# Performance work log

Measured on AMD Instinct MI355X. Metric: run time of the kernel, lower is better.

The kernel has to match this reference:

```python
import jax, jax.numpy as jnp
import numpy as np
from jax import lax

B, L, H, KSIZE = 8, 16384, 128, 65
PAD = KSIZE // 2  # 32; odd kernel keeps output length == L


def setup_inputs() -> dict:
    key = jax.random.key(0)
    kq, kk, kv, kw = jax.random.split(key, 4)
    Q = jax.random.normal(kq, (B, L, H), dtype=jnp.float32)
    K = jax.random.normal(kk, (B, L, H), dtype=jnp.float32)
    V = jax.random.normal(kv, (B, L, H), dtype=jnp.float32)
    # Conv1d weight [out_ch, in_ch, kernel], kaiming-like scale
    W = jax.random.normal(kw, (H, H, KSIZE), dtype=jnp.float32) / np.sqrt(H * KSIZE)
    return {"Q": Q, "K": K, "V": V, "W": W}


def reference(Q, K, V, W):
    # [B, L, H] -> [B, H, L] (channels-first, matching torch transpose(1,2))
    Qt = jnp.swapaxes(Q, 1, 2)
    Kt = jnp.swapaxes(K, 1, 2)
    Vt = jnp.swapaxes(V, 1, 2)
    # Conv1d over sequence dim; lax conv is cross-correlation like torch
    conv_q = lax.conv_general_dilated(
        Qt, W,
        window_strides=(1,),
        padding=[(PAD, PAD)],
        dimension_numbers=("NCH", "OIH", "NCH"),
    )  # [B, H, L]
    scores = conv_q * Kt                      # elementwise gate
    A = jax.nn.softmax(scores, axis=-1)       # softmax over sequence dim
    Z = A * Vt                                # weighted V (elementwise)
    return jnp.swapaxes(Z, 1, 2)              # back to [B, L, H]
```

## Files before the change

kernel.cpp:

```cpp
#include <hip/hip_runtime.h>
#include <stdint.h>

#define BATCH 8
#define LSEQ 16384
#define HDIM 128
#define KSZ 65
#define PADW 32
#define LH (LSEQ*HDIM)
#define TL 256
#define NROWS (TL + 2*PADW)
#define LBLKS (LSEQ/TL)
#define EXP_SHIFT 20.0f

#define WS_WBF_OFF 4096

typedef __attribute__((ext_vector_type(8))) short bf16x8;
typedef __attribute__((ext_vector_type(4))) short bf16x4;
typedef __attribute__((ext_vector_type(16))) float f32x16;

__device__ __forceinline__ unsigned short f2bf(float f) {
  unsigned int u = __float_as_uint(f);
  return (unsigned short)((u + 0x7FFFu + ((u >> 16) & 1u)) >> 16);
}

__global__ __launch_bounds__(256) void wcvt_kernel(const float* __restrict__ W,
                                                   unsigned short* __restrict__ Wbf) {
  __shared__ float lw[KSZ*HDIM];
  const int o = blockIdx.x;
  const float* src = W + (size_t)o * (HDIM*KSZ);
  for (int t = threadIdx.x; t < HDIM*KSZ; t += 256) lw[t] = src[t];
  __syncthreads();
  const int ob  = o >> 5;
  const int l31 = o & 31;
  for (int idx = threadIdx.x; idx < KSZ*HDIM; idx += 256) {
    const int k = idx >> 7;
    const int i = idx & 127;
    const int kk  = i >> 4;
    const int hi2 = (i >> 3) & 1;
    const int e   = i & 7;
    const size_t dst = ((((size_t)(k*4 + ob)*8 + kk)*2 + hi2)*32 + l31)*8 + e;
    Wbf[dst] = f2bf(lw[i*KSZ + k]);
  }
}

__global__ __launch_bounds__(512, 4) void conv_gate_kernel(
    const float* __restrict__ Qm, const float* __restrict__ Km,
    const unsigned short* __restrict__ Wfrag,
    float* __restrict__ Eout, float* __restrict__ gsum) {

  __shared__ __align__(16) unsigned short Qs[NROWS*HDIM];

  const int tid  = threadIdx.x;
  const int lane = tid & 63;
  const int w    = tid >> 6;
  const int wr   = w >> 1;
  const int wc   = w & 1;
  const int l31  = lane & 31;
  const int hi2  = lane >> 5;

  const int bx = blockIdx.x;
  const int b  = bx >> 6;
  const int l0 = (bx & 63) << 8;

  {
    const int r0 = tid >> 5;
    const int c4 = (tid & 31) << 2;
    const float* qbase = Qm + (size_t)b*LH + c4;
#pragma unroll
    for (int it = 0; it < NROWS/16; ++it) {
      const int r = it*16 + r0;
      const int grow = l0 - PADW + r;
      bf16x4 pk = {0, 0, 0, 0};
      if (grow >= 0 && grow < LSEQ) {
        const float4 qv = *(const float4*)(qbase + (size_t)grow*HDIM);
        pk[0] = (short)f2bf(qv.x); pk[1] = (short)f2bf(qv.y);
        pk[2] = (short)f2bf(qv.z); pk[3] = (short)f2bf(qv.w);
      }
      *(bf16x4*)(&Qs[r*HDIM + (c4 ^ ((r & 15) << 3))]) = pk;
    }
  }

  const unsigned short* pb = Wfrag + (size_t)(wc*2)*4096 + hi2*256 + l31*8;

  f32x16 acc[2][2] = {};

  __syncthreads();

  const int arow0 = wr*64 + l31;
  for (int k = 0; k < KSZ; ++k) {
    const unsigned short* pk = pb + (size_t)k*16384;
    const int r0 = k + arow0;
    const int r1 = r0 + 32;
    const int xa0 = (r0 & 15) << 3, xa1 = (r1 & 15) << 3;
#pragma unroll
    for (int kk = 0; kk < 8; ++kk) {
      const int i0 = kk*16 + hi2*8;
      const bf16x8 a0 = *(const bf16x8*)(&Qs[r0*HDIM + (i0 ^ xa0)]);
      const bf16x8 a1 = *(const bf16x8*)(&Qs[r1*HDIM + (i0 ^ xa1)]);
      const bf16x8 b0 = *(const bf16x8*)(pk + kk*512);
      const bf16x8 b1 = *(const bf16x8*)(pk + 4096 + kk*512);
      __builtin_amdgcn_s_setprio(1);
      acc[0][0] = __builtin_amdgcn_mfma_f32_32x32x16_bf16(a0, b0, acc[0][0], 0, 0, 0);
      acc[0][1] = __builtin_amdgcn_mfma_f32_32x32x16_bf16(a0, b1, acc[0][1], 0, 0, 0);
      acc[1][0] = __builtin_amdgcn_mfma_f32_32x32x16_bf16(a1, b0, acc[1][0], 0, 0, 0);
      acc[1][1] = __builtin_amdgcn_mfma_f32_32x32x16_bf16(a1, b1, acc[1][1], 0, 0, 0);
      __builtin_amdgcn_s_setprio(0);
    }
  }

  float psum[2] = {0.f, 0.f};
#pragma unroll
  for (int mf = 0; mf < 2; ++mf) {
#pragma unroll
    for (int r = 0; r < 16; ++r) {
      const int row = wr*64 + mf*32 + (r & 3) + 8*(r >> 2) + 4*hi2;
      const size_t gb = (size_t)b*LH + (size_t)(l0 + row)*HDIM + wc*64 + l31;
#pragma unroll
      for (int nf = 0; nf < 2; ++nf) {
        const float s = acc[mf][nf][r] * Km[gb + nf*32];
        const float e = __expf(s - EXP_SHIFT);
        Eout[gb + nf*32] = e;
        psum[nf] += e;
      }
    }
  }
  psum[0] += __shfl_xor(psum[0], 32);
  psum[1] += __shfl_xor(psum[1], 32);
  if (hi2 == 0) {
    atomicAdd(&gsum[b*HDIM + wc*64 + l31],      psum[0]);
    atomicAdd(&gsum[b*HDIM + wc*64 + 32 + l31], psum[1]);
  }
}

__global__ __launch_bounds__(256) void finalize_kernel(float* __restrict__ out,
                                                       const float* __restrict__ V,
                                                       const float* __restrict__ gsum) {
  const int total4 = (BATCH*LH) >> 2;
  const int stride = gridDim.x * blockDim.x;
  for (int f = blockIdx.x*blockDim.x + threadIdx.x; f < total4; f += stride) {
    const float4 e = ((const float4*)out)[f];
    const float4 v = ((const float4*)V)[f];
    const int e0 = f << 2;
    const float* gs = gsum + ((e0 >> 21) << 7) + (e0 & 127);
    float4 z;
    z.x = e.x * v.x / gs[0];
    z.y = e.y * v.y / gs[1];
    z.z = e.z * v.z / gs[2];
    z.w = e.w * v.w / gs[3];
    ((float4*)out)[f] = z;
  }
}

extern "C" void kernel_launch(void* const* d_in, const int* in_sizes, int n_in,
                              void* d_out, int out_size, void* d_ws, size_t ws_size,
                              hipStream_t stream) {
  (void)in_sizes; (void)n_in; (void)out_size; (void)ws_size;
  const float* Q = (const float*)d_in[0];
  const float* K = (const float*)d_in[1];
  const float* V = (const float*)d_in[2];
  const float* W = (const float*)d_in[3];
  float* out  = (float*)d_out;
  float* gsum = (float*)d_ws;
  unsigned short* Wbf = (unsigned short*)((char*)d_ws + WS_WBF_OFF);

  hipMemsetAsync(d_ws, 0, BATCH*HDIM*sizeof(float), stream);
  wcvt_kernel<<<HDIM, 256, 0, stream>>>(W, Wbf);
  conv_gate_kernel<<<BATCH*LBLKS, 512, 0, stream>>>(Q, K, Wbf, out, gsum);
  finalize_kernel<<<2048, 256, 0, stream>>>(out, V, gsum);
}
```

Measured before the change: 335.4 us.

## Stage conv weights into LDS with async global_load_lds ring buffer

Weight fragments were previously read straight from global memory by every wave on each tap. They are now streamed into a 4-slot LDS ring with direct global-to-LDS loads issued two phases ahead, with vmcnt waits and barriers between phases. The weight layout is reordered into half-k phases to suit this, and A/B fragments are batched in registers before the MFMAs. The goal is to cut redundant global/L2 traffic and hide load latency, at the cost of more LDS per block (occupancy hint drops from 4 to 2), a barrier every phase, and reliance on vmcnt ordering for correctness.

```diff
diff --git a/kernel.cpp b/kernel.cpp
--- a/kernel.cpp
+++ b/kernel.cpp
@@ -11,6 +11,8 @@
 #define NROWS (TL + 2*PADW)
 #define LBLKS (LSEQ/TL)
 #define EXP_SHIFT 20.0f
+#define NPH (2*KSZ)
+#define HB 8192
 
 #define WS_WBF_OFF 4096
 
@@ -36,19 +38,36 @@
     const int k = idx >> 7;
     const int i = idx & 127;
     const int kk  = i >> 4;
+    const int kkh = kk >> 2;
+    const int kk2 = kk & 3;
     const int hi2 = (i >> 3) & 1;
     const int e   = i & 7;
-    const size_t dst = ((((size_t)(k*4 + ob)*8 + kk)*2 + hi2)*32 + l31)*8 + e;
+    const size_t dst = (size_t)(k*2 + kkh)*HB + ob*2048 + kk2*512 + hi2*256 + l31*8 + e;
     Wbf[dst] = f2bf(lw[i*KSZ + k]);
   }
 }
 
-__global__ __launch_bounds__(512, 4) void conv_gate_kernel(
+__device__ __forceinline__ void stage_half(const unsigned short* __restrict__ Wbf, int ph,
+                                           unsigned short* dst, int w, int lane) {
+  const char* gbase = (const char*)(Wbf + (size_t)ph * HB);
+  char* lbase = (char*)dst;
+#pragma unroll
+  for (int r = 0; r < 2; ++r) {
+    const int off = r*8192 + w*1024;
+    __builtin_amdgcn_global_load_lds(
+        (const __attribute__((address_space(1))) unsigned int*)(gbase + off + lane*16),
+        (__attribute__((address_space(3))) unsigned int*)(lbase + off),
+        16, 0, 0);
+  }
+}
+
+__global__ __launch_bounds__(512, 2) void conv_gate_kernel(
     const float* __restrict__ Qm, const float* __restrict__ Km,
     const unsigned short* __restrict__ Wfrag,
     float* __restrict__ Eout, float* __restrict__ gsum) {
 
   __shared__ __align__(16) unsigned short Qs[NROWS*HDIM];
+  __shared__ __align__(16) unsigned short Ws[4*HB];
 
   const int tid  = threadIdx.x;
   const int lane = tid & 63;
@@ -80,31 +99,48 @@
     }
   }
 
-  const unsigned short* pb = Wfrag + (size_t)(wc*2)*4096 + hi2*256 + l31*8;
+  stage_half(Wfrag, 0, &Ws[0*HB], w, lane);
+  stage_half(Wfrag, 1, &Ws[1*HB], w, lane);
 
   f32x16 acc[2][2] = {};
 
   __syncthreads();
 
   const int arow0 = wr*64 + l31;
+  const int bo0 = (wc*2+0)*2048 + hi2*256 + l31*8;
+  const int bo1 = (wc*2+1)*2048 + hi2*256 + l31*8;
+
   for (int k = 0; k < KSZ; ++k) {
-    const unsigned short* pk = pb + (size_t)k*16384;
     const int r0 = k + arow0;
     const int r1 = r0 + 32;
     const int xa0 = (r0 & 15) << 3, xa1 = (r1 & 15) << 3;
 #pragma unroll
-    for (int kk = 0; kk < 8; ++kk) {
-      const int i0 = kk*16 + hi2*8;
-      const bf16x8 a0 = *(const bf16x8*)(&Qs[r0*HDIM + (i0 ^ xa0)]);
-      const bf16x8 a1 = *(const bf16x8*)(&Qs[r1*HDIM + (i0 ^ xa1)]);
-      const bf16x8 b0 = *(const bf16x8*)(pk + kk*512);
-      const bf16x8 b1 = *(const bf16x8*)(pk + 4096 + kk*512);
+    for (int kkh = 0; kkh < 2; ++kkh) {
+      const int p = k*2 + kkh;
+      asm volatile("s_waitcnt vmcnt(2)" ::: "memory");
+      if (p + 2 < NPH)
+        stage_half(Wfrag, p + 2, &Ws[((p + 2) & 3) * HB], w, lane);
+      const unsigned short* hb = &Ws[(p & 3) * HB];
+
+      bf16x8 a0[4], a1[4], b0[4], b1[4];
+#pragma unroll
+      for (int kk2 = 0; kk2 < 4; ++kk2) {
+        const int i0 = (kkh*4 + kk2)*16 + hi2*8;
+        a0[kk2] = *(const bf16x8*)(&Qs[r0*HDIM + (i0 ^ xa0)]);
+        a1[kk2] = *(const bf16x8*)(&Qs[r1*HDIM + (i0 ^ xa1)]);
+        b0[kk2] = *(const bf16x8*)(hb + bo0 + kk2*512);
+        b1[kk2] = *(const bf16x8*)(hb + bo1 + kk2*512);
+      }
       __builtin_amdgcn_s_setprio(1);
-      acc[0][0] = __builtin_amdgcn_mfma_f32_32x32x16_bf16(a0, b0, acc[0][0], 0, 0, 0);
-      acc[0][1] = __builtin_amdgcn_mfma_f32_32x32x16_bf16(a0, b1, acc[0][1], 0, 0, 0);
-      acc[1][0] = __builtin_amdgcn_mfma_f32_32x32x16_bf16(a1, b0, acc[1][0], 0, 0, 0);
-      acc[1][1] = __builtin_amdgcn_mfma_f32_32x32x16_bf16(a1, b1, acc[1][1], 0, 0, 0);
+#pragma unroll
+      for (int kk2 = 0; kk2 < 4; ++kk2) {
+        acc[0][0] = __builtin_amdgcn_mfma_f32_32x32x16_bf16(a0[kk2], b0[kk2], acc[0][0], 0, 0, 0);
+        acc[0][1] = __builtin_amdgcn_mfma_f32_32x32x16_bf16(a0[kk2], b1[kk2], acc[0][1], 0, 0, 0);
+        acc[1][0] = __builtin_amdgcn_mfma_f32_32x32x16_bf16(a1[kk2], b0[kk2], acc[1][0], 0, 0, 0);
+        acc[1][1] = __builtin_amdgcn_mfma_f32_32x32x16_bf16(a1[kk2], b1[kk2], acc[1][1], 0, 0, 0);
+      }
       __builtin_amdgcn_s_setprio(0);
+      __builtin_amdgcn_s_barrier();
     }
   }
 
```

Result: faster. 323.9 us (-3.4%).

## Stage conv weight taps into LDS with double-buffered async loads and split-K warps

Applied to the files above, without the earlier changes.

Weight fragments for each tap are now copied into a double-buffered LDS slot with global_load_lds, overlapping the next tap's load with the current tap's MFMAs. Previously each wave read them straight from global memory. The warp layout changes so each wave computes a 128x64 output tile over half of the input channels. The two halves are reduced through LDS before the exp and gate epilogue. This raises LDS use to 144 KB and lowers occupancy to 2 blocks, and it adds a barrier per tap.

```diff
diff --git a/kernel.cpp b/kernel.cpp
--- a/kernel.cpp
+++ b/kernel.cpp
@@ -11,6 +11,7 @@
 #define NROWS (TL + 2*PADW)
 #define LBLKS (LSEQ/TL)
 #define EXP_SHIFT 20.0f
+#define SLOT 16384
 
 #define WS_WBF_OFF 4096
 
@@ -38,23 +39,39 @@
     const int kk  = i >> 4;
     const int hi2 = (i >> 3) & 1;
     const int e   = i & 7;
-    const size_t dst = ((((size_t)(k*4 + ob)*8 + kk)*2 + hi2)*32 + l31)*8 + e;
+    const size_t dst = (size_t)k*SLOT + kk*2048 + ob*512 + hi2*256 + l31*8 + e;
     Wbf[dst] = f2bf(lw[i*KSZ + k]);
   }
 }
 
-__global__ __launch_bounds__(512, 4) void conv_gate_kernel(
+__device__ __forceinline__ void stage_tap(const unsigned short* __restrict__ gsrc,
+                                          char* lbase, int w, int lane) {
+  const char* gb = (const char*)gsrc;
+#pragma unroll
+  for (int r = 0; r < 4; ++r) {
+    const int off = r*8192 + w*1024;
+    __builtin_amdgcn_global_load_lds(
+        (const __attribute__((address_space(1))) unsigned int*)(gb + off + lane*16),
+        (__attribute__((address_space(3))) unsigned int*)(lbase + off),
+        16, 0, 0);
+  }
+}
+
+__global__ __launch_bounds__(512, 2) void conv_gate_kernel(
     const float* __restrict__ Qm, const float* __restrict__ Km,
     const unsigned short* __restrict__ Wfrag,
     float* __restrict__ Eout, float* __restrict__ gsum) {
 
-  __shared__ __align__(16) unsigned short Qs[NROWS*HDIM];
+  __shared__ __align__(16) char smem[147456];
+  unsigned short* Qs = (unsigned short*)smem;
+  char* WsBase = smem + 81920;
 
   const int tid  = threadIdx.x;
   const int lane = tid & 63;
   const int w    = tid >> 6;
-  const int wr   = w >> 1;
-  const int wc   = w & 1;
+  const int ks   = w & 1;
+  const int wc   = (w >> 1) & 1;
+  const int wr   = w >> 2;
   const int l31  = lane & 31;
   const int hi2  = lane >> 5;
 
@@ -80,55 +97,103 @@
     }
   }
 
-  const unsigned short* pb = Wfrag + (size_t)(wc*2)*4096 + hi2*256 + l31*8;
-
-  f32x16 acc[2][2] = {};
+  stage_tap(Wfrag, WsBase, w, lane);
+
+  f32x16 acc[4][2] = {};
 
   __syncthreads();
 
-  const int arow0 = wr*64 + l31;
+  const int arow0 = wr*128 + l31;
+  const int bbase = (wc*2)*512 + lane*8;
+
+#define LOADC(c, A0,A1,A2,A3,B0,B1) { \
+    const int i0 = (ks*64 + (c)*16 + hi2*8) ^ xa; \
+    A0 = *(const bf16x8*)(&Qs[(rb     )*HDIM + i0]); \
+    A1 = *(const bf16x8*)(&Qs[(rb + 32)*HDIM + i0]); \
+    A2 = *(const bf16x8*)(&Qs[(rb + 64)*HDIM + i0]); \
+    A3 = *(const bf16x8*)(&Qs[(rb + 96)*HDIM + i0]); \
+    B0 = *(const bf16x8*)(&slot[(ks*4 + (c))*2048 + bbase]); \
+    B1 = *(const bf16x8*)(&slot[(ks*4 + (c))*2048 + bbase + 512]); \
+  }
+#define MM(A0,A1,A2,A3,B0,B1) \
+    acc[0][0] = __builtin_amdgcn_mfma_f32_32x32x16_bf16(A0, B0, acc[0][0], 0, 0, 0); \
+    acc[0][1] = __builtin_amdgcn_mfma_f32_32x32x16_bf16(A0, B1, acc[0][1], 0, 0, 0); \
+    acc[1][0] = __builtin_amdgcn_mfma_f32_32x32x16_bf16(A1, B0, acc[1][0], 0, 0, 0); \
+    acc[1][1] = __builtin_amdgcn_mfma_f32_32x32x16_bf16(A1, B1, acc[1][1], 0, 0, 0); \
+    acc[2][0] = __builtin_amdgcn_mfma_f32_32x32x16_bf16(A2, B0, acc[2][0], 0, 0, 0); \
+    acc[2][1] = __builtin_amdgcn_mfma_f32_32x32x16_bf16(A2, B1, acc[2][1], 0, 0, 0); \
+    acc[3][0] = __builtin_amdgcn_mfma_f32_32x32x16_bf16(A3, B0, acc[3][0], 0, 0, 0); \
+    acc[3][1] = __builtin_amdgcn_mfma_f32_32x32x16_bf16(A3, B1, acc[3][1], 0, 0, 0);
+
   for (int k = 0; k < KSZ; ++k) {
-    const unsigned short* pk = pb + (size_t)k*16384;
-    const int r0 = k + arow0;
-    const int r1 = r0 + 32;
-    const int xa0 = (r0 & 15) << 3, xa1 = (r1 & 15) << 3;
-#pragma unroll
-    for (int kk = 0; kk < 8; ++kk) {
-      const int i0 = kk*16 + hi2*8;
-      const bf16x8 a0 = *(const bf16x8*)(&Qs[r0*HDIM + (i0 ^ xa0)]);
-      const bf16x8 a1 = *(const bf16x8*)(&Qs[r1*HDIM + (i0 ^ xa1)]);
-      const bf16x8 b0 = *(const bf16x8*)(pk + kk*512);
-      const bf16x8 b1 = *(const bf16x8*)(pk + 4096 + kk*512);
-      __builtin_amdgcn_s_setprio(1);
-      acc[0][0] = __builtin_amdgcn_mfma_f32_32x32x16_bf16(a0, b0, acc[0][0], 0, 0, 0);
-      acc[0][1] = __builtin_amdgcn_mfma_f32_32x32x16_bf16(a0, b1, acc[0][1], 0, 0, 0);
-      acc[1][0] = __builtin_amdgcn_mfma_f32_32x32x16_bf16(a1, b0, acc[1][0], 0, 0, 0);
-      acc[1][1] = __builtin_amdgcn_mfma_f32_32x32x16_bf16(a1, b1, acc[1][1], 0, 0, 0);
-      __builtin_amdgcn_s_setprio(0);
-    }
-  }
-
-  float psum[2] = {0.f, 0.f};
-#pragma unroll
-  for (int mf = 0; mf < 2; ++mf) {
-#pragma unroll
-    for (int r = 0; r < 16; ++r) {
-      const int row = wr*64 + mf*32 + (r & 3) + 8*(r >> 2) + 4*hi2;
-      const size_t gb = (size_t)b*LH + (size_t)(l0 + row)*HDIM + wc*64 + l31;
-#pragma unroll
-      for (int nf = 0; nf < 2; ++nf) {
-        const float s = acc[mf][nf][r] * Km[gb + nf*32];
-        const float e = __expf(s - EXP_SHIFT);
-        Eout[gb + nf*32] = e;
-        psum[nf] += e;
+    const unsigned short* slot = (const unsigned short*)(WsBase + (k & 1)*32768);
+    if (k < KSZ-1)
+      stage_tap(Wfrag + (size_t)(k+1)*SLOT, WsBase + ((k+1) & 1)*32768, w, lane);
+
+    const int rb = k + arow0;
+    const int xa = (rb & 15) << 3;
+
+    bf16x8 a0,a1,a2,a3,b0,b1, c0,c1,c2,c3,d0,d1;
+    LOADC(0, a0,a1,a2,a3,b0,b1)
+    LOADC(1, c0,c1,c2,c3,d0,d1)
+    MM(a0,a1,a2,a3,b0,b1)
+    LOADC(2, a0,a1,a2,a3,b0,b1)
+    MM(c0,c1,c2,c3,d0,d1)
+    LOADC(3, c0,c1,c2,c3,d0,d1)
+    MM(a0,a1,a2,a3,b0,b1)
+    MM(c0,c1,c2,c3,d0,d1)
+
+    asm volatile("s_waitcnt vmcnt(0)" ::: "memory");
+    __builtin_amdgcn_s_barrier();
+  }
+#undef LOADC
+#undef MM
+
+  float* red = (float*)smem;
+  const int widx = wr*2 + wc;
+  float* reg = red + widx*8192 + lane*4;
+  if (ks == 1) {
+#pragma unroll
+    for (int e4 = 0; e4 < 32; ++e4) {
+      const int mfr = e4 >> 3, nf = (e4 >> 2) & 1, r4 = (e4 & 3) << 2;
+      float4 v;
+      v.x = acc[mfr][nf][r4];   v.y = acc[mfr][nf][r4+1];
+      v.z = acc[mfr][nf][r4+2]; v.w = acc[mfr][nf][r4+3];
+      *(float4*)(reg + e4*256) = v;
+    }
+  }
+  __syncthreads();
+
+  if (ks == 0) {
+#pragma unroll
+    for (int e4 = 0; e4 < 32; ++e4) {
+      const int mfr = e4 >> 3, nf = (e4 >> 2) & 1, r4 = (e4 & 3) << 2;
+      const float4 v = *(const float4*)(reg + e4*256);
+      acc[mfr][nf][r4]   += v.x; acc[mfr][nf][r4+1] += v.y;
+      acc[mfr][nf][r4+2] += v.z; acc[mfr][nf][r4+3] += v.w;
+    }
+    float psum[2] = {0.f, 0.f};
+#pragma unroll
+    for (int mfr = 0; mfr < 4; ++mfr) {
+#pragma unroll
+      for (int r = 0; r < 16; ++r) {
+        const int row = wr*128 + mfr*32 + (r & 3) + 8*(r >> 2) + 4*hi2;
+        const size_t gb = (size_t)b*LH + (size_t)(l0 + row)*HDIM + wc*64 + l31;
+#pragma unroll
+        for (int nf = 0; nf < 2; ++nf) {
+          const float s = acc[mfr][nf][r] * Km[gb + nf*32];
+          const float e = __expf(s - EXP_SHIFT);
+          Eout[gb + nf*32] = e;
+          psum[nf] += e;
+        }
       }
     }
-  }
-  psum[0] += __shfl_xor(psum[0], 32);
-  psum[1] += __shfl_xor(psum[1], 32);
-  if (hi2 == 0) {
-    atomicAdd(&gsum[b*HDIM + wc*64 + l31],      psum[0]);
-    atomicAdd(&gsum[b*HDIM + wc*64 + 32 + l31], psum[1]);
+    psum[0] += __shfl_xor(psum[0], 32);
+    psum[1] += __shfl_xor(psum[1], 32);
+    if (hi2 == 0) {
+      atomicAdd(&gsum[b*HDIM + wc*64 + l31],      psum[0]);
+      atomicAdd(&gsum[b*HDIM + wc*64 + 32 + l31], psum[1]);
+    }
   }
 }
 
```

After: 279.9 us (median of 2 runs). -16.5%, faster.

## Stage conv weights into LDS with double-buffered async loads and split-K waves

Applied to the files above, without the earlier changes.

Each wave used to read the bf16 weight fragments straight from global memory inside the 65-tap loop. Now the weights are repacked into half-tap slots and streamed into a double-buffered LDS area with global_load_lds, prefetching the next slot while MFMAs run on the current one. The sequence tile shrinks from 256 to 128 rows, and the 8 waves split the reduction dimension in two, with the partial accumulators combined through LDS before the exp/gate epilogue. This adds a barrier per phase (130 phases) and about 80KB of LDS per block, which limits occupancy, and it doubles the number of blocks and the redundant Q halo loads.

```diff
diff --git a/kernel.cpp b/kernel.cpp
--- a/kernel.cpp
+++ b/kernel.cpp
@@ -7,10 +7,12 @@
 #define KSZ 65
 #define PADW 32
 #define LH (LSEQ*HDIM)
-#define TL 256
+#define TL 128
 #define NROWS (TL + 2*PADW)
 #define LBLKS (LSEQ/TL)
 #define EXP_SHIFT 20.0f
+#define HSLOT 8192
+#define NPH (2*KSZ)
 
 #define WS_WBF_OFF 4096
 
@@ -35,11 +37,25 @@
   for (int idx = threadIdx.x; idx < KSZ*HDIM; idx += 256) {
     const int k = idx >> 7;
     const int i = idx & 127;
-    const int kk  = i >> 4;
+    const int hk  = i >> 6;
+    const int kq  = (i >> 4) & 3;
     const int hi2 = (i >> 3) & 1;
     const int e   = i & 7;
-    const size_t dst = ((((size_t)(k*4 + ob)*8 + kk)*2 + hi2)*32 + l31)*8 + e;
+    const size_t dst = (size_t)(k*2 + hk)*HSLOT + kq*2048 + ob*512 + hi2*256 + l31*8 + e;
     Wbf[dst] = f2bf(lw[i*KSZ + k]);
+  }
+}
+
+__device__ __forceinline__ void stage_half(const unsigned short* __restrict__ gsrc,
+                                           char* lbase, int w, int lane) {
+  const char* gb = (const char*)gsrc;
+#pragma unroll
+  for (int r = 0; r < 2; ++r) {
+    const int off = r*8192 + w*1024;
+    __builtin_amdgcn_global_load_lds(
+        (const __attribute__((address_space(1))) unsigned int*)(gb + off + lane*16),
+        (__attribute__((address_space(3))) unsigned int*)(lbase + off),
+        16, 0, 0);
   }
 }
 
@@ -48,19 +64,22 @@
     const unsigned short* __restrict__ Wfrag,
     float* __restrict__ Eout, float* __restrict__ gsum) {
 
-  __shared__ __align__(16) unsigned short Qs[NROWS*HDIM];
+  __shared__ __align__(16) char smem[81920];
+  unsigned short* Qs = (unsigned short*)smem;
+  char* WsBase = smem + NROWS*HDIM*2;
 
   const int tid  = threadIdx.x;
   const int lane = tid & 63;
   const int w    = tid >> 6;
-  const int wr   = w >> 1;
-  const int wc   = w & 1;
+  const int ks   = w & 1;
+  const int wc   = (w >> 1) & 1;
+  const int wr   = w >> 2;
   const int l31  = lane & 31;
   const int hi2  = lane >> 5;
 
   const int bx = blockIdx.x;
-  const int b  = bx >> 6;
-  const int l0 = (bx & 63) << 8;
+  const int b  = bx >> 7;
+  const int l0 = (bx & 127) << 7;
 
   {
     const int r0 = tid >> 5;
@@ -80,55 +99,91 @@
     }
   }
 
-  const unsigned short* pb = Wfrag + (size_t)(wc*2)*4096 + hi2*256 + l31*8;
+  stage_half(Wfrag, WsBase, w, lane);
 
   f32x16 acc[2][2] = {};
 
   __syncthreads();
 
   const int arow0 = wr*64 + l31;
-  for (int k = 0; k < KSZ; ++k) {
-    const unsigned short* pk = pb + (size_t)k*16384;
-    const int r0 = k + arow0;
-    const int r1 = r0 + 32;
-    const int xa0 = (r0 & 15) << 3, xa1 = (r1 & 15) << 3;
-#pragma unroll
-    for (int kk = 0; kk < 8; ++kk) {
-      const int i0 = kk*16 + hi2*8;
-      const bf16x8 a0 = *(const bf16x8*)(&Qs[r0*HDIM + (i0 ^ xa0)]);
-      const bf16x8 a1 = *(const bf16x8*)(&Qs[r1*HDIM + (i0 ^ xa1)]);
-      const bf16x8 b0 = *(const bf16x8*)(pk + kk*512);
-      const bf16x8 b1 = *(const bf16x8*)(pk + 4096 + kk*512);
-      __builtin_amdgcn_s_setprio(1);
-      acc[0][0] = __builtin_amdgcn_mfma_f32_32x32x16_bf16(a0, b0, acc[0][0], 0, 0, 0);
-      acc[0][1] = __builtin_amdgcn_mfma_f32_32x32x16_bf16(a0, b1, acc[0][1], 0, 0, 0);
-      acc[1][0] = __builtin_amdgcn_mfma_f32_32x32x16_bf16(a1, b0, acc[1][0], 0, 0, 0);
-      acc[1][1] = __builtin_amdgcn_mfma_f32_32x32x16_bf16(a1, b1, acc[1][1], 0, 0, 0);
-      __builtin_amdgcn_s_setprio(0);
-    }
-  }
-
-  float psum[2] = {0.f, 0.f};
-#pragma unroll
-  for (int mf = 0; mf < 2; ++mf) {
-#pragma unroll
-    for (int r = 0; r < 16; ++r) {
-      const int row = wr*64 + mf*32 + (r & 3) + 8*(r >> 2) + 4*hi2;
-      const size_t gb = (size_t)b*LH + (size_t)(l0 + row)*HDIM + wc*64 + l31;
-#pragma unroll
-      for (int nf = 0; nf < 2; ++nf) {
-        const float s = acc[mf][nf][r] * Km[gb + nf*32];
-        const float e = __expf(s - EXP_SHIFT);
-        Eout[gb + nf*32] = e;
-        psum[nf] += e;
+  const int bB = (wc*2)*512 + hi2*256 + l31*8;
+
+  for (int p = 0; p < NPH; ++p) {
+    if (p + 1 < NPH)
+      stage_half(Wfrag + (size_t)(p+1)*HSLOT, WsBase + ((p+1) & 1)*16384, w, lane);
+    const unsigned short* slot = (const unsigned short*)(WsBase + (p & 1)*16384);
+    const int k  = p >> 1;
+    const int hk = p & 1;
+    const int rb = k + arow0, rb2 = rb + 32;
+    const int xa = (rb & 15) << 3, xa2 = (rb2 & 15) << 3;
+
+    bf16x8 A0[2], A1[2], B0[2], B1[2];
+#pragma unroll
+    for (int c = 0; c < 2; ++c) {
+      const int i0 = hk*64 + (ks*2 + c)*16 + hi2*8;
+      A0[c] = *(const bf16x8*)(&Qs[rb *HDIM + (i0 ^ xa )]);
+      A1[c] = *(const bf16x8*)(&Qs[rb2*HDIM + (i0 ^ xa2)]);
+      B0[c] = *(const bf16x8*)(slot + (ks*2 + c)*2048 + bB);
+      B1[c] = *(const bf16x8*)(slot + (ks*2 + c)*2048 + bB + 512);
+    }
+    __builtin_amdgcn_s_setprio(1);
+#pragma unroll
+    for (int c = 0; c < 2; ++c) {
+      acc[0][0] = __builtin_amdgcn_mfma_f32_32x32x16_bf16(A0[c], B0[c], acc[0][0], 0, 0, 0);
+      acc[0][1] = __builtin_amdgcn_mfma_f32_32x32x16_bf16(A0[c], B1[c], acc[0][1], 0, 0, 0);
+      acc[1][0] = __builtin_amdgcn_mfma_f32_32x32x16_bf16(A1[c], B0[c], acc[1][0], 0, 0, 0);
+      acc[1][1] = __builtin_amdgcn_mfma_f32_32x32x16_bf16(A1[c], B1[c], acc[1][1], 0, 0, 0);
+    }
+    __builtin_amdgcn_s_setprio(0);
+    asm volatile("s_waitcnt vmcnt(0)" ::: "memory");
+    __builtin_amdgcn_s_barrier();
+  }
+
+  float* red = (float*)smem;
+  const int widx = wr*2 + wc;
+  float* reg = red + widx*4096 + lane*4;
+  if (ks == 1) {
+#pragma unroll
+    for (int q = 0; q < 16; ++q) {
+      const int mf = q >> 3, nf = (q >> 2) & 1, r4 = (q & 3) << 2;
+      float4 v;
+      v.x = acc[mf][nf][r4];   v.y = acc[mf][nf][r4+1];
+      v.z = acc[mf][nf][r4+2]; v.w = acc[mf][nf][r4+3];
+      *(float4*)(reg + q*256) = v;
+    }
+  }
+  __syncthreads();
+
+  if (ks == 0) {
+#pragma unroll
+    for (int q = 0; q < 16; ++q) {
+      const int mf = q >> 3, nf = (q >> 2) & 1, r4 = (q & 3) << 2;
+      const float4 v = *(const float4*)(reg + q*256);
+      acc[mf][nf][r4]   += v.x; acc[mf][nf][r4+1] += v.y;
+      acc[mf][nf][r4+2] += v.z; acc[mf][nf][r4+3] += v.w;
+    }
+    float psum[2] = {0.f, 0.f};
+#pragma unroll
+    for (int mf = 0; mf < 2; ++mf) {
+#pragma unroll
+      for (int r = 0; r < 16; ++r) {
+        const int row = wr*64 + mf*32 + (r & 3) + 8*(r >> 2) + 4*hi2;
+        const size_t gb = (size_t)b*LH + (size_t)(l0 + row)*HDIM + wc*64 + l31;
+#pragma unroll
+        for (int nf = 0; nf < 2; ++nf) {
+          const float s = acc[mf][nf][r] * Km[gb + nf*32];
+          const float e = __expf(s - EXP_SHIFT);
+          Eout[gb + nf*32] = e;
+          psum[nf] += e;
+        }
       }
     }
-  }
-  psum[0] += __shfl_xor(psum[0], 32);
-  psum[1] += __shfl_xor(psum[1], 32);
-  if (hi2 == 0) {
-    atomicAdd(&gsum[b*HDIM + wc*64 + l31],      psum[0]);
-    atomicAdd(&gsum[b*HDIM + wc*64 + 32 + l31], psum[1]);
+    psum[0] += __shfl_xor(psum[0], 32);
+    psum[1] += __shfl_xor(psum[1], 32);
+    if (hi2 == 0) {
+      atomicAdd(&gsum[b*HDIM + wc*64 + l31],      psum[0]);
+      atomicAdd(&gsum[b*HDIM + wc*64 + 32 + l31], psum[1]);
+    }
   }
 }
 
```

Measured after the change: 299.3 us. -10.8%, faster.
